# Performance work log

Measured on AMD Instinct MI355X. Metric: run time of the kernel, lower is better.

Reference implementation:

```python
import jax, jax.numpy as jnp
from jax import lax
import numpy as np

H, W_DIM = 4096, 4096
KH, KW = 2, 2


def setup_inputs() -> dict:
    key = jax.random.key(0)
    kx, kw = jax.random.split(key)
    X = jax.random.normal(kx, (H, W_DIM), dtype=jnp.float32)
    W = jax.random.uniform(kw, (KH, KW), dtype=jnp.float32)
    return {"X": X, "W": W}


def _conv_valid(X, W):
    # VALID 2D cross-correlation: Y[i,j] = sum_{a,b} X[i+a, j+b] * W[a,b]
    x = X[None, None]          # [1,1,H,W]
    k = W[None, None]          # [1,1,kh,kw]
    y = lax.conv_general_dilated(x, k, window_strides=(1, 1), padding='VALID')
    return y[0, 0]             # [H-kh+1, W-kw+1]


def _trans_conv(X, W):
    # Transposed conv (scatter-add of X[i,j]*W) == full *convolution* with W,
    # i.e. cross-correlation with the spatially flipped kernel, padding kh-1/kw-1.
    x = X[None, None]
    k = W[::-1, ::-1][None, None]
    y = lax.conv_general_dilated(x, k, window_strides=(1, 1),
                                 padding=[(KH - 1, KH - 1), (KW - 1, KW - 1)])
    return y[0, 0]             # back to [H, W]


def reference(X, W):
    y1 = _conv_valid(X, W)     # [H-1, W-1]
    y2 = _trans_conv(y1, W)    # [H, W]
    return y2
```

## Files before the change

kernel.cpp:

```cpp
#include <hip/hip_runtime.h>


#define HD 4096
#define QPR 1024
#define RB 8

__device__ __forceinline__ void load_row(const float* __restrict__ X, int row,
                                         int j0, float x[6]) {
    if (row >= 0 && row < HD) {
        const float* rp = X + (size_t)row * HD;
        const float4 v = *reinterpret_cast<const float4*>(rp + j0);
        x[1] = v.x; x[2] = v.y; x[3] = v.z; x[4] = v.w;
        x[0] = (j0 > 0)      ? rp[j0 - 1] : 0.f;
        x[5] = (j0 + 4 < HD) ? rp[j0 + 4] : 0.f;
    } else {
        #pragma unroll
        for (int c = 0; c < 6; ++c) x[c] = 0.f;
    }
}

__global__ __launch_bounds__(256) void fused_conv_kernel(
    const float* __restrict__ X, const float* __restrict__ Wk,
    float* __restrict__ Y)
{
    const int idx  = blockIdx.x * blockDim.x + threadIdx.x;
    const int i0   = (idx >> 10) * RB;
    const int j0   = (idx & (QPR - 1)) << 2;

    const float w00 = Wk[0], w01 = Wk[1], w10 = Wk[2], w11 = Wk[3];

    bool qv[5];
    #pragma unroll
    for (int q = 0; q < 5; ++q) {
        const int qc = j0 - 1 + q;
        qv[q] = (qc >= 0) && (qc < HD - 1);
    }

    float xa[6], xb[6];
    load_row(X, i0 - 1, j0, xa);
    load_row(X, i0,     j0, xb);

    float y1p[5];
    {
        const bool pv = (i0 - 1 >= 0);
        #pragma unroll
        for (int q = 0; q < 5; ++q) {
            const float v = w00 * xa[q] + w01 * xa[q + 1]
                          + w10 * xb[q] + w11 * xb[q + 1];
            y1p[q] = (pv && qv[q]) ? v : 0.f;
        }
    }

    #pragma unroll
    for (int r = 0; r < RB; ++r) {
        const int i = i0 + r;
        load_row(X, i + 1, j0, xa);

        float y1c[5];
        const bool pv = (i < HD - 1);
        #pragma unroll
        for (int q = 0; q < 5; ++q) {
            const float v = w00 * xb[q] + w01 * xb[q + 1]
                          + w10 * xa[q] + w11 * xa[q + 1];
            y1c[q] = (pv && qv[q]) ? v : 0.f;
        }

        float4 out;
        out.x = w00 * y1c[1] + w01 * y1c[0] + w10 * y1p[1] + w11 * y1p[0];
        out.y = w00 * y1c[2] + w01 * y1c[1] + w10 * y1p[2] + w11 * y1p[1];
        out.z = w00 * y1c[3] + w01 * y1c[2] + w10 * y1p[3] + w11 * y1p[2];
        out.w = w00 * y1c[4] + w01 * y1c[3] + w10 * y1p[4] + w11 * y1p[3];
        *reinterpret_cast<float4*>(Y + (size_t)i * HD + j0) = out;

        #pragma unroll
        for (int q = 0; q < 5; ++q) y1p[q] = y1c[q];
        #pragma unroll
        for (int c = 0; c < 6; ++c) xb[c] = xa[c];
    }
}

extern "C" void kernel_launch(void* const* d_in, const int* in_sizes, int n_in,
                              void* d_out, int out_size, void* d_ws, size_t ws_size,
                              hipStream_t stream) {
    const float* X  = (const float*)d_in[0];
    const float* Wk = (const float*)d_in[1];
    float* Y        = (float*)d_out;

    const int total_threads = (HD / RB) * QPR;
    const int block = 256;
    const int grid  = total_threads / block;
    fused_conv_kernel<<<grid, block, 0, stream>>>(X, Wk, Y);
}
```

Before: 120.1 us.

## Share halo columns via wave shuffles, preload all rows, use nontemporal stores

Each thread now gets its left and right halo values from neighbouring lanes with shuffles instead of two extra scalar global loads per row. Only the wave-edge lanes fetch from memory. All RB+2 input rows are loaded up front so more loads are in flight at once, and outputs are written with nontemporal stores to avoid polluting the cache. The cost is higher register pressure from the preloaded row array, plus shuffle instructions.

Measured after the change: 116.1 us. -3.4%, faster.

```diff
diff --git a/kernel.cpp b/kernel.cpp
--- a/kernel.cpp
+++ b/kernel.cpp
@@ -5,19 +5,7 @@
 #define QPR 1024
 #define RB 8
 
-__device__ __forceinline__ void load_row(const float* __restrict__ X, int row,
-                                         int j0, float x[6]) {
-    if (row >= 0 && row < HD) {
-        const float* rp = X + (size_t)row * HD;
-        const float4 v = *reinterpret_cast<const float4*>(rp + j0);
-        x[1] = v.x; x[2] = v.y; x[3] = v.z; x[4] = v.w;
-        x[0] = (j0 > 0)      ? rp[j0 - 1] : 0.f;
-        x[5] = (j0 + 4 < HD) ? rp[j0 + 4] : 0.f;
-    } else {
-        #pragma unroll
-        for (int c = 0; c < 6; ++c) x[c] = 0.f;
-    }
-}
+typedef float f32x4 __attribute__((ext_vector_type(4)));
 
 __global__ __launch_bounds__(256) void fused_conv_kernel(
     const float* __restrict__ X, const float* __restrict__ Wk,
@@ -26,56 +14,69 @@
     const int idx  = blockIdx.x * blockDim.x + threadIdx.x;
     const int i0   = (idx >> 10) * RB;
     const int j0   = (idx & (QPR - 1)) << 2;
+    const int lane = threadIdx.x & 63;
 
     const float w00 = Wk[0], w01 = Wk[1], w10 = Wk[2], w11 = Wk[3];
 
-    bool qv[5];
+    float x[RB + 2][6];
     #pragma unroll
-    for (int q = 0; q < 5; ++q) {
-        const int qc = j0 - 1 + q;
-        qv[q] = (qc >= 0) && (qc < HD - 1);
+    for (int r = 0; r < RB + 2; ++r) {
+        const int row = i0 - 1 + r;
+        if (row >= 0 && row < HD) {
+            const float* rp = X + (size_t)row * HD;
+            const f32x4 v = *reinterpret_cast<const f32x4*>(rp + j0);
+            float lft = __shfl_up(v[3], 1);
+            float rgt = __shfl_down(v[0], 1);
+            const int  eoff = (lane == 0) ? (j0 - 1) : (j0 + 4);
+            const bool need = ((lane == 0) || (lane == 63)) &&
+                              (eoff >= 0) && (eoff < HD);
+            const float ev  = need ? rp[eoff] : 0.f;
+            if (lane == 0)  lft = ev;
+            if (lane == 63) rgt = ev;
+            x[r][0] = lft;  x[r][1] = v[0]; x[r][2] = v[1];
+            x[r][3] = v[2]; x[r][4] = v[3]; x[r][5] = rgt;
+        } else {
+            #pragma unroll
+            for (int c = 0; c < 6; ++c) x[r][c] = 0.f;
+        }
     }
 
-    float xa[6], xb[6];
-    load_row(X, i0 - 1, j0, xa);
-    load_row(X, i0,     j0, xb);
+    const bool lv = (j0 > 0);
+    const bool rv = (j0 + 4 < HD);
 
-    float y1p[5];
+    float y1p[5], y1c[5];
     {
-        const bool pv = (i0 - 1 >= 0);
+        const bool pv = (i0 > 0);
         #pragma unroll
         for (int q = 0; q < 5; ++q) {
-            const float v = w00 * xa[q] + w01 * xa[q + 1]
-                          + w10 * xb[q] + w11 * xb[q + 1];
-            y1p[q] = (pv && qv[q]) ? v : 0.f;
+            const float v = w00 * x[0][q] + w01 * x[0][q + 1]
+                          + w10 * x[1][q] + w11 * x[1][q + 1];
+            const bool ok = pv && (q != 0 || lv) && (q != 4 || rv);
+            y1p[q] = ok ? v : 0.f;
         }
     }
 
     #pragma unroll
     for (int r = 0; r < RB; ++r) {
         const int i = i0 + r;
-        load_row(X, i + 1, j0, xa);
-
-        float y1c[5];
         const bool pv = (i < HD - 1);
         #pragma unroll
         for (int q = 0; q < 5; ++q) {
-            const float v = w00 * xb[q] + w01 * xb[q + 1]
-                          + w10 * xa[q] + w11 * xa[q + 1];
-            y1c[q] = (pv && qv[q]) ? v : 0.f;
+            const float v = w00 * x[r + 1][q] + w01 * x[r + 1][q + 1]
+                          + w10 * x[r + 2][q] + w11 * x[r + 2][q + 1];
+            const bool ok = pv && (q != 0 || lv) && (q != 4 || rv);
+            y1c[q] = ok ? v : 0.f;
         }
 
-        float4 out;
-        out.x = w00 * y1c[1] + w01 * y1c[0] + w10 * y1p[1] + w11 * y1p[0];
-        out.y = w00 * y1c[2] + w01 * y1c[1] + w10 * y1p[2] + w11 * y1p[1];
-        out.z = w00 * y1c[3] + w01 * y1c[2] + w10 * y1p[3] + w11 * y1p[2];
-        out.w = w00 * y1c[4] + w01 * y1c[3] + w10 * y1p[4] + w11 * y1p[3];
-        *reinterpret_cast<float4*>(Y + (size_t)i * HD + j0) = out;
+        f32x4 o;
+        o[0] = w00 * y1c[1] + w01 * y1c[0] + w10 * y1p[1] + w11 * y1p[0];
+        o[1] = w00 * y1c[2] + w01 * y1c[1] + w10 * y1p[2] + w11 * y1p[1];
+        o[2] = w00 * y1c[3] + w01 * y1c[2] + w10 * y1p[3] + w11 * y1p[2];
+        o[3] = w00 * y1c[4] + w01 * y1c[3] + w10 * y1p[4] + w11 * y1p[3];
+        __builtin_nontemporal_store(o, reinterpret_cast<f32x4*>(Y + (size_t)i * HD + j0));
 
         #pragma unroll
         for (int q = 0; q < 5; ++q) y1p[q] = y1c[q];
-        #pragma unroll
-        for (int c = 0; c < 6; ++c) xb[c] = xa[c];
     }
 }
 
```
